# Kernel tuning notes

Measured on AMD Instinct MI355X. Metric: run time of the kernel, lower is better.

Reference implementation:

```python
import jax, jax.numpy as jnp
import numpy as np

SCORE_THRESHOLD = 0.5
IOU_THRESHOLD = 0.5
N = 8192
IMG = 640.0


def setup_inputs() -> dict:
    key = jax.random.key(0)
    k1, k2, k3 = jax.random.split(key, 3)
    # valid xyxy boxes on a 640px canvas: x2 > x1, y2 > y1
    xy1 = jax.random.uniform(k1, (N, 2), dtype=jnp.float32) * (IMG - 64.0)
    wh = jax.random.uniform(k2, (N, 2), dtype=jnp.float32) * 96.0 + 4.0
    xyxy = jnp.concatenate([xy1, xy1 + wh], axis=1)  # [N,4]
    person_conf = jax.random.uniform(k3, (N,), dtype=jnp.float32)  # [N]
    return {"xyxy": xyxy, "person_conf": person_conf}


def _pairwise_iou(boxes):
    # boxes: [N,4] xyxy -> iou: [N,N]
    x1, y1, x2, y2 = boxes[:, 0], boxes[:, 1], boxes[:, 2], boxes[:, 3]
    area = (x2 - x1) * (y2 - y1)  # [N]
    ix1 = jnp.maximum(x1[:, None], x1[None, :])
    iy1 = jnp.maximum(y1[:, None], y1[None, :])
    ix2 = jnp.minimum(x2[:, None], x2[None, :])
    iy2 = jnp.minimum(y2[:, None], y2[None, :])
    iw = jnp.maximum(ix2 - ix1, 0.0)
    ih = jnp.maximum(iy2 - iy1, 0.0)
    inter = iw * ih
    union = area[:, None] + area[None, :] - inter
    return inter / jnp.maximum(union, 1e-9)


def reference(xyxy, person_conf):
    # score-threshold filter (as a mask to stay jit-compatible / fixed shape)
    valid = person_conf >= SCORE_THRESHOLD  # [N]
    # sort by score descending; invalid boxes sink to the bottom
    sort_scores = jnp.where(valid, person_conf, -jnp.inf)
    order = jnp.argsort(-sort_scores)  # [N]
    boxes_s = xyxy[order]              # [N,4]
    scores_s = person_conf[order]      # [N]
    valid_s = valid[order]             # [N]

    iou = _pairwise_iou(boxes_s)  # [N,N]
    idx = jnp.arange(N)

    def body(i, keep):
        # box i (if still kept) suppresses lower-scored overlapping boxes
        sup = keep[i] & (iou[i] > IOU_THRESHOLD) & (idx > i)
        return keep & ~sup

    keep = jax.lax.fori_loop(0, N, body, valid_s)  # [N] bool

    boxes_and_scores = jnp.concatenate([boxes_s, scores_s[:, None]], axis=1)  # [N,5]
    out = jnp.where(keep[:, None], boxes_and_scores, 0.0)  # suppressed rows zeroed
    return out, keep
```

## Files before the change

kernel.cpp:

```cpp
#include <hip/hip_runtime.h>

typedef unsigned long long u64;
typedef unsigned int u32;

static constexpr int N = 8192;
static constexpr int NW = N / 64;
static constexpr int RSEG = 32;
static constexpr int CAPW = 512;
static constexpr int ECAP = 10240;


__device__ __forceinline__ u64 make_key(float s, int i) {
  u32 adj = (s >= 0.5f) ? (__float_as_uint(s) + 1u) : 0u;
  return ((u64)adj << 32) | (u64)(u32)(N - 1 - i);
}

__global__ __launch_bounds__(256)
void rank_kernel(const float* __restrict__ conf, u32* __restrict__ rank_partial,
                 u32* __restrict__ cntG, u64* __restrict__ validmG,
                 int* __restrict__ nvG) {
  __shared__ u64 sk[256];
  const int t = threadIdx.x;
  if (blockIdx.x == 0 && blockIdx.y == 0) {
    if (t < NW) { cntG[t] = 0; validmG[t] = 0; }
    if (t == 0) *nvG = 0;
  }
  const int jb = blockIdx.y;
  const int j = jb * 256 + t;
  sk[t] = make_key(conf[j], j);
  __syncthreads();
  const int i = blockIdx.x * 256 + t;
  const u64 ki = make_key(conf[i], i);
  int cnt = 0;
  #pragma unroll 8
  for (int k = 0; k < 256; ++k) cnt += (sk[k] > ki);
  rank_partial[jb * N + i] = (u32)cnt;
}

__global__ __launch_bounds__(256)
void scatter_kernel(const float4* __restrict__ xyxy, const float* __restrict__ conf,
                    const u32* __restrict__ rank_partial,
                    float4* __restrict__ boxes_s, float* __restrict__ scores_s,
                    float* __restrict__ areas_s, u64* __restrict__ validmG,
                    int* __restrict__ nvG) {
  #pragma clang fp contract(off)
  const int i = blockIdx.x * 256 + threadIdx.x;
  u32 r = 0;
  #pragma unroll
  for (int jb = 0; jb < RSEG; ++jb) r += rank_partial[jb * N + i];
  float4 b = xyxy[i];
  float c = conf[i];
  boxes_s[r] = b;
  scores_s[r] = c;
  areas_s[r] = (b.z - b.x) * (b.w - b.y);
  if (c >= 0.5f) {
    atomicOr(&validmG[r >> 6], 1ull << (r & 63));
    atomicAdd(nvG, 1);
  }
}

__global__ __launch_bounds__(256)
void mask_kernel(const float4* __restrict__ boxes_s, const float* __restrict__ areas_s,
                 const float* __restrict__ scores_s,
                 uint4* __restrict__ edge4, u32* __restrict__ cntG,
                 u64* __restrict__ Dg) {
  #pragma clang fp contract(off)
  __shared__ float4 cb[4][64];
  __shared__ float ca[4][64];
  const int wave = threadIdx.x >> 6;
  const int t = threadIdx.x & 63;
  const int xb = blockIdx.x * 4 + wave;
  const int yb = blockIdx.y;
  if (xb < yb) return;
  if (scores_s[xb * 64] < 0.5f) return;
  cb[wave][t] = boxes_s[xb * 64 + t];
  ca[wave][t] = areas_s[xb * 64 + t];
  const int i = yb * 64 + t;
  const float4 rb = boxes_s[i];
  const float ra = areas_s[i];
  const float sc_i = scores_s[i];
  const int jbase = xb * 64;
  u64 w = 0;
  for (int q = 0; q < 64; ++q) {
    float4 c = cb[wave][q];
    float ix1 = fmaxf(rb.x, c.x);
    float iy1 = fmaxf(rb.y, c.y);
    float ix2 = fminf(rb.z, c.z);
    float iy2 = fminf(rb.w, c.w);
    float iw = fmaxf(ix2 - ix1, 0.0f);
    float ih = fmaxf(iy2 - iy1, 0.0f);
    float inter = iw * ih;
    float uni = fmaxf((ra + ca[wave][q]) - inter, 1e-9f);
    float iou = inter / uni;
    if ((iou > 0.5f) && (jbase + q > i)) w |= (1ull << q);
  }
  if (sc_i < 0.5f) w = 0;
  if (xb == yb) {
    Dg[(u64)yb * 64 + t] = w;
    return;
  }
  u64 nz = __ballot(w != 0ull);
  if (!nz) return;
  int base = 0;
  if (t == 0) base = atomicAdd(&cntG[yb], (u32)__popcll(nz));
  base = __shfl(base, 0);
  if (w) {
    int idx = base + __popcll(nz & ((1ull << t) - 1ull));
    if (idx < CAPW) {
      edge4[(u64)yb * CAPW + idx] =
          make_uint4((u32)w, (u32)(w >> 32), (u32)i | ((u32)xb << 16), 0u);
    }
  }
}

__global__ __launch_bounds__(256, 1)
void sweep_kernel(const uint4* __restrict__ edge4, const u32* __restrict__ cntG,
                  const u64* __restrict__ validmG, const int* __restrict__ nvG,
                  const u64* __restrict__ Dg, u64* __restrict__ keepmG) {
  __shared__ u64 maskL[ECAP];
  __shared__ u32 metaL[ECAP];
  __shared__ u32 offL[NW + 1];
  __shared__ u64 keepL[NW];
  __shared__ u32 rem32[2 * NW];
  __shared__ u32 cntL[NW];
  const int tid = threadIdx.x;
  const int wv = tid >> 6;
  const int t = tid & 63;

  if (tid < NW) { cntL[tid] = min(cntG[tid], (u32)CAPW); keepL[tid] = 0; }
  rem32[tid] = 0;
  __syncthreads();

  if (tid < 64) {
    u32 a = cntL[t];
    u32 b = cntL[64 + t];
    #pragma unroll
    for (int d = 1; d < 64; d <<= 1) { u32 n = __shfl_up(a, d); if (t >= d) a += n; }
    u32 tot = __shfl(a, 63);
    #pragma unroll
    for (int d = 1; d < 64; d <<= 1) { u32 n = __shfl_up(b, d); if (t >= d) b += n; }
    b += tot;
    a = min(a, (u32)ECAP);
    b = min(b, (u32)ECAP);
    if (t == 0) offL[0] = 0;
    offL[1 + t] = a;
    offL[65 + t] = b;
  }
  __syncthreads();

  for (int w = wv; w < NW; w += 4) {
    u32 o = offL[w];
    u32 ce = offL[w + 1] - o;
    const uint4* src = edge4 + (u64)w * CAPW;
    for (u32 s = t; s < ce; s += 64) {
      uint4 r = src[s];
      maskL[o + s] = ((u64)r.y << 32) | (u64)r.x;
      metaL[o + s] = r.z;
    }
  }
  __syncthreads();

  if (tid < 64) {
    const int NWv = min((*nvG + 63) >> 6, NW);
    if (NWv > 0) {
      u64 vr0 = validmG[t];
      u64 vr1 = validmG[64 + t];
      u32 or0 = offL[t];
      u32 or1 = offL[64 + t];
      u32 or2 = offL[128];
      u64 dc = Dg[t];
      u64 dn = Dg[(u64)((NWv > 1) ? 1 : 0) * 64 + t];

      for (int y = 0; y < NWv; ++y) {
        int yp = (y + 2 < NWv) ? (y + 2) : (NWv - 1);
        u64 dnn = Dg[(u64)yp * 64 + t];
        u32 o  = (y < 64) ? __shfl(or0, y) : __shfl(or1, y - 64);
        u32 oe = (y + 1 < 64) ? __shfl(or0, y + 1)
               : (y + 1 < 128) ? __shfl(or1, y + 1 - 64) : or2;
        u32 ce = oe - o;
        u32 meta0 = 0, meta1 = 0, meta2 = 0, meta3 = 0;
        u64 m0 = 0, m1 = 0, m2 = 0, m3 = 0;
        if (t < ce)       { meta0 = metaL[o + t];       m0 = maskL[o + t]; }
        if (64 + t < ce)  { meta1 = metaL[o + 64 + t];  m1 = maskL[o + 64 + t]; }
        if (128 + t < ce) { meta2 = metaL[o + 128 + t]; m2 = maskL[o + 128 + t]; }
        if (192 + t < ce) { meta3 = metaL[o + 192 + t]; m3 = maskL[o + 192 + t]; }
        u32 r0 = rem32[2 * y];
        u32 r1 = rem32[2 * y + 1];
        u64 vv = (y < 64) ? __shfl(vr0, y) : __shfl(vr1, y - 64);
        u64 kk = vv & ~(((u64)r1 << 32) | (u64)r0);
        u64 im = __ballot(dc != 0ull) & kk;
        while (im) {
          int q = __ffsll((long long)im) - 1;
          u64 dq = __shfl(dc, q);
          kk &= ~dq;
          im &= ~(1ull << q);
          im &= kk;
        }
        if (t == 0) keepL[y] = kk;
        if (t < ce && ((kk >> (meta0 & 63u)) & 1ull)) {
          u32 x = meta0 >> 16;
          atomicOr(&rem32[2 * x], (u32)m0);
          atomicOr(&rem32[2 * x + 1], (u32)(m0 >> 32));
        }
        if (64 + t < ce && ((kk >> (meta1 & 63u)) & 1ull)) {
          u32 x = meta1 >> 16;
          atomicOr(&rem32[2 * x], (u32)m1);
          atomicOr(&rem32[2 * x + 1], (u32)(m1 >> 32));
        }
        if (128 + t < ce && ((kk >> (meta2 & 63u)) & 1ull)) {
          u32 x = meta2 >> 16;
          atomicOr(&rem32[2 * x], (u32)m2);
          atomicOr(&rem32[2 * x + 1], (u32)(m2 >> 32));
        }
        if (192 + t < ce && ((kk >> (meta3 & 63u)) & 1ull)) {
          u32 x = meta3 >> 16;
          atomicOr(&rem32[2 * x], (u32)m3);
          atomicOr(&rem32[2 * x + 1], (u32)(m3 >> 32));
        }
        for (u32 s = 256 + t; s < ce; s += 64) {
          u32 meta = metaL[o + s];
          u64 m = maskL[o + s];
          if ((kk >> (meta & 63u)) & 1ull) {
            u32 x = meta >> 16;
            atomicOr(&rem32[2 * x], (u32)m);
            atomicOr(&rem32[2 * x + 1], (u32)(m >> 32));
          }
        }
        dc = dn;
        dn = dnn;
      }
    }
  }
  __syncthreads();
  if (tid < NW) keepmG[tid] = keepL[tid];
}

__global__ __launch_bounds__(256)
void writeout_kernel(const u64* __restrict__ keepmG,
                     const float4* __restrict__ boxes_s,
                     const float* __restrict__ scores_s,
                     float* __restrict__ out) {
  const int s = blockIdx.x * 256 + threadIdx.x;
  bool keep = (keepmG[s >> 6] >> (s & 63)) & 1ull;
  float4 b = boxes_s[s];
  float sc = scores_s[s];
  float* row = out + (u64)s * 5;
  if (keep) {
    row[0] = b.x; row[1] = b.y; row[2] = b.z; row[3] = b.w; row[4] = sc;
    out[N * 5 + s] = 1.0f;
  } else {
    row[0] = 0.0f; row[1] = 0.0f; row[2] = 0.0f; row[3] = 0.0f; row[4] = 0.0f;
    out[N * 5 + s] = 0.0f;
  }
}

extern "C" void kernel_launch(void* const* d_in, const int* in_sizes, int n_in,
                              void* d_out, int out_size, void* d_ws, size_t ws_size,
                              hipStream_t stream) {
  const float4* xyxy = (const float4*)d_in[0];
  const float* conf  = (const float*)d_in[1];
  char* ws = (char*)d_ws;
  float4* boxes_s   = (float4*)(ws + 0);
  float*  scores_s  = (float*)(ws + 131072);
  float*  areas_s   = (float*)(ws + 163840);
  u32*    cntG      = (u32*)(ws + 196608);
  int*    nvG       = (int*)(ws + 197120);
  u64*    validmG   = (u64*)(ws + 197184);
  u64*    keepmG    = (u64*)(ws + 198208);
  u64*    Dg        = (u64*)(ws + 199680);
  uint4*  edge4     = (uint4*)(ws + 265216);
  u32*    rank_partial = (u32*)(ws + 1313792);
  float*  out       = (float*)d_out;

  dim3 rg(N / 256, RSEG);
  rank_kernel<<<rg, 256, 0, stream>>>(conf, rank_partial, cntG, validmG, nvG);
  scatter_kernel<<<N / 256, 256, 0, stream>>>(xyxy, conf, rank_partial,
                                              boxes_s, scores_s, areas_s,
                                              validmG, nvG);
  dim3 mg(NW / 4, NW);
  mask_kernel<<<mg, 256, 0, stream>>>(boxes_s, areas_s, scores_s,
                                      edge4, cntG, Dg);
  sweep_kernel<<<1, 256, 0, stream>>>(edge4, cntG, validmG, nvG, Dg, keepmG);
  writeout_kernel<<<N / 256, 256, 0, stream>>>(keepmG, boxes_s, scores_s, out);
}
```

Before: 140.2 us.

## Fold diagonal-block masks into sparse edge list and use 64-bit LDS atomics in sweep

Diagonal 64x64 IoU blocks are no longer written to a dense Dg array. They go into the same compacted edge list as off-diagonal blocks, and the sweep pulls the intra-block suppression masks from that list using wave-wide OR reductions. The edge-list copy into LDS becomes a flat loop that finds each row block by binary search, and the paired 32-bit removal atomics become single 64-bit LDS atomicOr operations. In exchange, the serial greedy loop now runs a 12-step shuffle reduction for every kept candidate, where it used to do one shuffle, which may lengthen the single-block critical path.

Result: slower. 163.4 us (+16.6%).

```diff
diff --git a/kernel.cpp b/kernel.cpp
--- a/kernel.cpp
+++ b/kernel.cpp
@@ -13,6 +13,16 @@
 __device__ __forceinline__ u64 make_key(float s, int i) {
   u32 adj = (s >= 0.5f) ? (__float_as_uint(s) + 1u) : 0u;
   return ((u64)adj << 32) | (u64)(u32)(N - 1 - i);
+}
+
+__device__ __forceinline__ u64 wave_or_u64(u64 v) {
+  u32 lo = (u32)v, hi = (u32)(v >> 32);
+  #pragma unroll
+  for (int d = 1; d < 64; d <<= 1) {
+    lo |= __shfl_xor(lo, d);
+    hi |= __shfl_xor(hi, d);
+  }
+  return ((u64)hi << 32) | (u64)lo;
 }
 
 __global__ __launch_bounds__(256)
@@ -62,8 +72,7 @@
 __global__ __launch_bounds__(256)
 void mask_kernel(const float4* __restrict__ boxes_s, const float* __restrict__ areas_s,
                  const float* __restrict__ scores_s,
-                 uint4* __restrict__ edge4, u32* __restrict__ cntG,
-                 u64* __restrict__ Dg) {
+                 uint4* __restrict__ edge4, u32* __restrict__ cntG) {
   #pragma clang fp contract(off)
   __shared__ float4 cb[4][64];
   __shared__ float ca[4][64];
@@ -95,10 +104,6 @@
     if ((iou > 0.5f) && (jbase + q > i)) w |= (1ull << q);
   }
   if (sc_i < 0.5f) w = 0;
-  if (xb == yb) {
-    Dg[(u64)yb * 64 + t] = w;
-    return;
-  }
   u64 nz = __ballot(w != 0ull);
   if (!nz) return;
   int base = 0;
@@ -116,19 +121,21 @@
 __global__ __launch_bounds__(256, 1)
 void sweep_kernel(const uint4* __restrict__ edge4, const u32* __restrict__ cntG,
                   const u64* __restrict__ validmG, const int* __restrict__ nvG,
-                  const u64* __restrict__ Dg, u64* __restrict__ keepmG) {
+                  u64* __restrict__ keepmG) {
   __shared__ u64 maskL[ECAP];
   __shared__ u32 metaL[ECAP];
   __shared__ u32 offL[NW + 1];
+  __shared__ u64 rem64[NW];
   __shared__ u64 keepL[NW];
-  __shared__ u32 rem32[2 * NW];
   __shared__ u32 cntL[NW];
   const int tid = threadIdx.x;
-  const int wv = tid >> 6;
   const int t = tid & 63;
 
-  if (tid < NW) { cntL[tid] = min(cntG[tid], (u32)CAPW); keepL[tid] = 0; }
-  rem32[tid] = 0;
+  if (tid < NW) {
+    cntL[tid] = min(cntG[tid], (u32)CAPW);
+    rem64[tid] = 0;
+    keepL[tid] = 0;
+  }
   __syncthreads();
 
   if (tid < 64) {
@@ -148,86 +155,97 @@
   }
   __syncthreads();
 
-  for (int w = wv; w < NW; w += 4) {
-    u32 o = offL[w];
-    u32 ce = offL[w + 1] - o;
-    const uint4* src = edge4 + (u64)w * CAPW;
-    for (u32 s = t; s < ce; s += 64) {
-      uint4 r = src[s];
-      maskL[o + s] = ((u64)r.y << 32) | (u64)r.x;
-      metaL[o + s] = r.z;
+  const u32 T = offL[NW];
+  for (u32 s = tid; s < T; s += 256) {
+    int lo = 0, hi = NW;
+    #pragma unroll
+    for (int it = 0; it < 7; ++it) {
+      int mid = (lo + hi) >> 1;
+      if (offL[mid] <= s) lo = mid; else hi = mid;
     }
+    uint4 r = edge4[(u64)lo * CAPW + (s - offL[lo])];
+    maskL[s] = ((u64)r.y << 32) | (u64)r.x;
+    metaL[s] = r.z;
   }
   __syncthreads();
 
   if (tid < 64) {
     const int NWv = min((*nvG + 63) >> 6, NW);
-    if (NWv > 0) {
-      u64 vr0 = validmG[t];
-      u64 vr1 = validmG[64 + t];
-      u32 or0 = offL[t];
-      u32 or1 = offL[64 + t];
-      u32 or2 = offL[128];
-      u64 dc = Dg[t];
-      u64 dn = Dg[(u64)((NWv > 1) ? 1 : 0) * 64 + t];
-
-      for (int y = 0; y < NWv; ++y) {
-        int yp = (y + 2 < NWv) ? (y + 2) : (NWv - 1);
-        u64 dnn = Dg[(u64)yp * 64 + t];
-        u32 o  = (y < 64) ? __shfl(or0, y) : __shfl(or1, y - 64);
-        u32 oe = (y + 1 < 64) ? __shfl(or0, y + 1)
-               : (y + 1 < 128) ? __shfl(or1, y + 1 - 64) : or2;
-        u32 ce = oe - o;
-        u32 meta0 = 0, meta1 = 0, meta2 = 0, meta3 = 0;
-        u64 m0 = 0, m1 = 0, m2 = 0, m3 = 0;
-        if (t < ce)       { meta0 = metaL[o + t];       m0 = maskL[o + t]; }
-        if (64 + t < ce)  { meta1 = metaL[o + 64 + t];  m1 = maskL[o + 64 + t]; }
-        if (128 + t < ce) { meta2 = metaL[o + 128 + t]; m2 = maskL[o + 128 + t]; }
-        if (192 + t < ce) { meta3 = metaL[o + 192 + t]; m3 = maskL[o + 192 + t]; }
-        u32 r0 = rem32[2 * y];
-        u32 r1 = rem32[2 * y + 1];
-        u64 vv = (y < 64) ? __shfl(vr0, y) : __shfl(vr1, y - 64);
-        u64 kk = vv & ~(((u64)r1 << 32) | (u64)r0);
-        u64 im = __ballot(dc != 0ull) & kk;
-        while (im) {
-          int q = __ffsll((long long)im) - 1;
-          u64 dq = __shfl(dc, q);
-          kk &= ~dq;
-          im &= ~(1ull << q);
-          im &= kk;
-        }
-        if (t == 0) keepL[y] = kk;
-        if (t < ce && ((kk >> (meta0 & 63u)) & 1ull)) {
-          u32 x = meta0 >> 16;
-          atomicOr(&rem32[2 * x], (u32)m0);
-          atomicOr(&rem32[2 * x + 1], (u32)(m0 >> 32));
-        }
-        if (64 + t < ce && ((kk >> (meta1 & 63u)) & 1ull)) {
-          u32 x = meta1 >> 16;
-          atomicOr(&rem32[2 * x], (u32)m1);
-          atomicOr(&rem32[2 * x + 1], (u32)(m1 >> 32));
-        }
-        if (128 + t < ce && ((kk >> (meta2 & 63u)) & 1ull)) {
-          u32 x = meta2 >> 16;
-          atomicOr(&rem32[2 * x], (u32)m2);
-          atomicOr(&rem32[2 * x + 1], (u32)(m2 >> 32));
-        }
-        if (192 + t < ce && ((kk >> (meta3 & 63u)) & 1ull)) {
-          u32 x = meta3 >> 16;
-          atomicOr(&rem32[2 * x], (u32)m3);
-          atomicOr(&rem32[2 * x + 1], (u32)(m3 >> 32));
-        }
-        for (u32 s = 256 + t; s < ce; s += 64) {
-          u32 meta = metaL[o + s];
-          u64 m = maskL[o + s];
-          if ((kk >> (meta & 63u)) & 1ull) {
-            u32 x = meta >> 16;
-            atomicOr(&rem32[2 * x], (u32)m);
-            atomicOr(&rem32[2 * x + 1], (u32)(m >> 32));
-          }
-        }
-        dc = dn;
-        dn = dnn;
+    u32 vlo0 = (u32)validmG[t],        vhi0 = (u32)(validmG[t] >> 32);
+    u32 vlo1 = (u32)validmG[64 + t],   vhi1 = (u32)(validmG[64 + t] >> 32);
+    u32 or0 = offL[t];
+    u32 or1 = offL[64 + t];
+    u32 or2 = offL[128];
+
+    for (int y = 0; y < NWv; ++y) {
+      u32 o  = (y < 64) ? __shfl(or0, y) : __shfl(or1, y - 64);
+      u32 oe = (y + 1 < 64) ? __shfl(or0, y + 1)
+             : (y + 1 < 128) ? __shfl(or1, y + 1 - 64) : or2;
+      u32 ce = oe - o;
+      u64 rm = rem64[y];
+      u32 mt0 = 0, mt1 = 0, mt2 = 0, mt3 = 0, mt4 = 0, mt5 = 0, mt6 = 0, mt7 = 0;
+      u64 mm0 = 0, mm1 = 0, mm2 = 0, mm3 = 0, mm4 = 0, mm5 = 0, mm6 = 0, mm7 = 0;
+      bool v0 = (u32)t < ce, v1 = 64u + t < ce, v2 = 128u + t < ce, v3 = 192u + t < ce;
+      bool v4 = false, v5 = false, v6 = false, v7 = false;
+      if (v0) { mt0 = metaL[o + t];        mm0 = maskL[o + t]; }
+      if (v1) { mt1 = metaL[o + 64 + t];   mm1 = maskL[o + 64 + t]; }
+      if (v2) { mt2 = metaL[o + 128 + t];  mm2 = maskL[o + 128 + t]; }
+      if (v3) { mt3 = metaL[o + 192 + t];  mm3 = maskL[o + 192 + t]; }
+      if (ce > 256) {
+        v4 = 256u + t < ce; v5 = 320u + t < ce; v6 = 384u + t < ce; v7 = 448u + t < ce;
+        if (v4) { mt4 = metaL[o + 256 + t]; mm4 = maskL[o + 256 + t]; }
+        if (v5) { mt5 = metaL[o + 320 + t]; mm5 = maskL[o + 320 + t]; }
+        if (v6) { mt6 = metaL[o + 384 + t]; mm6 = maskL[o + 384 + t]; }
+        if (v7) { mt7 = metaL[o + 448 + t]; mm7 = maskL[o + 448 + t]; }
+      }
+      bool i0 = v0 && (mt0 >> 16) == (u32)y;
+      bool i1 = v1 && (mt1 >> 16) == (u32)y;
+      bool i2 = v2 && (mt2 >> 16) == (u32)y;
+      bool i3 = v3 && (mt3 >> 16) == (u32)y;
+      bool i4 = v4 && (mt4 >> 16) == (u32)y;
+      bool i5 = v5 && (mt5 >> 16) == (u32)y;
+      bool i6 = v6 && (mt6 >> 16) == (u32)y;
+      bool i7 = v7 && (mt7 >> 16) == (u32)y;
+      u64 c = 0;
+      if (i0) c |= 1ull << (mt0 & 63u);
+      if (i1) c |= 1ull << (mt1 & 63u);
+      if (i2) c |= 1ull << (mt2 & 63u);
+      if (i3) c |= 1ull << (mt3 & 63u);
+      if (i4) c |= 1ull << (mt4 & 63u);
+      if (i5) c |= 1ull << (mt5 & 63u);
+      if (i6) c |= 1ull << (mt6 & 63u);
+      if (i7) c |= 1ull << (mt7 & 63u);
+      u64 imAll = wave_or_u64(c);
+      u32 vl = (y < 64) ? __shfl(vlo0, y) : __shfl(vlo1, y - 64);
+      u32 vh = (y < 64) ? __shfl(vhi0, y) : __shfl(vhi1, y - 64);
+      u64 kk = (((u64)vh << 32) | (u64)vl) & ~rm;
+      u64 im = imAll & kk;
+      while (im) {
+        int q = __ffsll((long long)im) - 1;
+        u64 dsel = 0;
+        if (i0 && (int)(mt0 & 63u) == q) dsel |= mm0;
+        if (i1 && (int)(mt1 & 63u) == q) dsel |= mm1;
+        if (i2 && (int)(mt2 & 63u) == q) dsel |= mm2;
+        if (i3 && (int)(mt3 & 63u) == q) dsel |= mm3;
+        if (i4 && (int)(mt4 & 63u) == q) dsel |= mm4;
+        if (i5 && (int)(mt5 & 63u) == q) dsel |= mm5;
+        if (i6 && (int)(mt6 & 63u) == q) dsel |= mm6;
+        if (i7 && (int)(mt7 & 63u) == q) dsel |= mm7;
+        u64 dq = wave_or_u64(dsel);
+        kk &= ~dq;
+        im &= ~(1ull << q);
+        im &= kk;
+      }
+      if (t == 0) keepL[y] = kk;
+      if (v0 && ((kk >> (mt0 & 63u)) & 1ull)) atomicOr(&rem64[mt0 >> 16], mm0);
+      if (v1 && ((kk >> (mt1 & 63u)) & 1ull)) atomicOr(&rem64[mt1 >> 16], mm1);
+      if (v2 && ((kk >> (mt2 & 63u)) & 1ull)) atomicOr(&rem64[mt2 >> 16], mm2);
+      if (v3 && ((kk >> (mt3 & 63u)) & 1ull)) atomicOr(&rem64[mt3 >> 16], mm3);
+      if (ce > 256) {
+        if (v4 && ((kk >> (mt4 & 63u)) & 1ull)) atomicOr(&rem64[mt4 >> 16], mm4);
+        if (v5 && ((kk >> (mt5 & 63u)) & 1ull)) atomicOr(&rem64[mt5 >> 16], mm5);
+        if (v6 && ((kk >> (mt6 & 63u)) & 1ull)) atomicOr(&rem64[mt6 >> 16], mm6);
+        if (v7 && ((kk >> (mt7 & 63u)) & 1ull)) atomicOr(&rem64[mt7 >> 16], mm7);
       }
     }
   }
@@ -267,7 +285,6 @@
   int*    nvG       = (int*)(ws + 197120);
   u64*    validmG   = (u64*)(ws + 197184);
   u64*    keepmG    = (u64*)(ws + 198208);
-  u64*    Dg        = (u64*)(ws + 199680);
   uint4*  edge4     = (uint4*)(ws + 265216);
   u32*    rank_partial = (u32*)(ws + 1313792);
   float*  out       = (float*)d_out;
@@ -278,8 +295,7 @@
                                               boxes_s, scores_s, areas_s,
                                               validmG, nvG);
   dim3 mg(NW / 4, NW);
-  mask_kernel<<<mg, 256, 0, stream>>>(boxes_s, areas_s, scores_s,
-                                      edge4, cntG, Dg);
-  sweep_kernel<<<1, 256, 0, stream>>>(edge4, cntG, validmG, nvG, Dg, keepmG);
+  mask_kernel<<<mg, 256, 0, stream>>>(boxes_s, areas_s, scores_s, edge4, cntG);
+  sweep_kernel<<<1, 256, 0, stream>>>(edge4, cntG, validmG, nvG, keepmG);
   writeout_kernel<<<N / 256, 256, 0, stream>>>(keepmG, boxes_s, scores_s, out);
 }
```
